# Optimization experiments

Hardware: AMD Instinct MI355X
Metric: run time of the kernel (lower is better)

The kernel has to match this reference:

```python
import jax, jax.numpy as jnp
import numpy as np

COMMITMENT_COST = 0.25


def setup_inputs() -> dict:
    key = jax.random.key(0)
    k1, k2 = jax.random.split(key)
    B, S, D, K = 16, 4096, 256, 4096
    inputs = jax.random.normal(k1, (B, S, D), dtype=jnp.float32)
    # codebook ~ embedding.weight (init scale irrelevant for correctness baseline)
    codebook = jax.random.normal(k2, (K, D), dtype=jnp.float32)
    return {"inputs": inputs, "codebook": codebook}


def reference(inputs, codebook):
    B, S, D = inputs.shape
    flat = inputs.reshape(-1, D)  # (N, D)
    distances = (
        jnp.sum(flat * flat, axis=1, keepdims=True)
        + jnp.sum(codebook * codebook, axis=1)
        - 2.0 * jnp.matmul(flat, codebook.T)
    )
    encoding_indices = jnp.argmin(distances, axis=1)  # (N,)
    quantized = codebook[encoding_indices].reshape(inputs.shape)  # gather
    # commitment loss: beta * mse(inputs, sg(quantized))
    diff = inputs - jax.lax.stop_gradient(quantized)
    commitment_loss = COMMITMENT_COST * jnp.mean(diff * diff)
    # straight-through estimator
    quantized_st = inputs + jax.lax.stop_gradient(quantized - inputs)
    return quantized_st, commitment_loss, encoding_indices
```

## Files before the change

### kernel.cpp

```cpp
#include <hip/hip_runtime.h>
#include <stdint.h>

typedef _Float16 half8 __attribute__((ext_vector_type(8)));
typedef float f32x4 __attribute__((ext_vector_type(4)));

#define DDIM 256
#define KCODES 4096
#define BM 128
#define BN 256
#define NCH 8
#define STEPS 128
#define DELTA 0.02f
#define FLT_BIG 3.4e38f

#define GLOAD_LDS(gsrc, ldst)                                                        \
    __builtin_amdgcn_global_load_lds(                                                \
        (const __attribute__((address_space(1))) void*)(const void*)(gsrc),          \
        (__attribute__((address_space(3))) void*)(void*)(ldst), 16, 0, 0)

__global__ void cvt_hl_kernel(const float* __restrict__ src, half8* __restrict__ dst) {
    int gid = blockIdx.x * 256 + threadIdx.x;
    int p = gid & 7;
    int ch = (gid >> 3) & 7;
    long row = gid >> 6;
    int part = p >> 2, quad = p & 3;
    const float* s = src + row * DDIM + ch * 32 + quad * 8;
    half8 h;
    #pragma unroll
    for (int j = 0; j < 8; ++j) {
        float v = s[j];
        _Float16 hi = (_Float16)v;
        h[j] = part ? (_Float16)(v - (float)hi) : hi;
    }
    dst[gid] = h;
}

__global__ void enorm_kernel(const float* __restrict__ cb, float* __restrict__ en, int K) {
    int gid = blockIdx.x * blockDim.x + threadIdx.x;
    int code = gid >> 6;
    int lane = threadIdx.x & 63;
    if (code >= K) return;
    const float4 v = *reinterpret_cast<const float4*>(&cb[(size_t)code * DDIM + lane * 4]);
    float s = v.x * v.x + v.y * v.y + v.z * v.z + v.w * v.w;
    #pragma unroll
    for (int off = 32; off > 0; off >>= 1) s += __shfl_xor(s, off, 64);
    if (lane == 0) en[code] = s;
}

__global__ __launch_bounds__(512, 2)
void vq_mfma_kernel(const half8* x16, const half8* __restrict__ cb16,
                    const float* __restrict__ en, const float* __restrict__ x,
                    const float* __restrict__ cb, float* out,
                    int* __restrict__ list, int* __restrict__ counter,
                    float* __restrict__ loss_accum, int N) {
    __shared__ __align__(16) half8 Abuf[2][BM * 8];
    __shared__ __align__(16) half8 Bbuf[2][BN * 8];
    __shared__ float en_lds[KCODES];
    __shared__ float red_d[4][BM];
    __shared__ float red_d2[4][BM];
    __shared__ int   red_i[4][BM];
    __shared__ int   binfo[BM];
    __shared__ float wsum[8];

    const int tid = threadIdx.x;
    const int lane = tid & 63;
    const int w = tid >> 6;
    const int wr = w >> 2, wc = w & 3;
    const int l15 = lane & 15, l4 = lane >> 4;
    const int brow = blockIdx.x * BM;
    const size_t ND = (size_t)N * DDIM;

    ((float4*)en_lds)[tid] = ((const float4*)en)[tid];
    ((float4*)en_lds)[tid + 512] = ((const float4*)en)[tid + 512];

    const int lrow = lane >> 3;
    const int swz = (lane & 7) ^ lrow;
    const half8* pA0 = x16 + ((size_t)(brow + w * 8       + lrow) * NCH) * 8 + swz;
    const half8* pA1 = x16 + ((size_t)(brow + (w + 8) * 8 + lrow) * NCH) * 8 + swz;
    const half8* pB0 = cb16 + ((size_t)((w     ) * 8 + lrow) * NCH) * 8 + swz;
    const half8* pB1 = cb16 + ((size_t)((w +  8) * 8 + lrow) * NCH) * 8 + swz;
    const half8* pB2 = cb16 + ((size_t)((w + 16) * 8 + lrow) * NCH) * 8 + swz;
    const half8* pB3 = cb16 + ((size_t)((w + 24) * 8 + lrow) * NCH) * 8 + swz;

#define STAGE(b_) do {                                      \
        GLOAD_LDS(pA0, &Abuf[b_][(w     ) * 64]);           \
        GLOAD_LDS(pA1, &Abuf[b_][(w +  8) * 64]);           \
        GLOAD_LDS(pB0, &Bbuf[b_][(w     ) * 64]);           \
        GLOAD_LDS(pB1, &Bbuf[b_][(w +  8) * 64]);           \
        GLOAD_LDS(pB2, &Bbuf[b_][(w + 16) * 64]);           \
        GLOAD_LDS(pB3, &Bbuf[b_][(w + 24) * 64]);           \
    } while (0)

#define ADVANCE(roll_) do {                                 \
        const int dA = (roll_) ? -56 : 8;                   \
        const int dB = (roll_) ? 16328 : 8;                 \
        pA0 += dA; pA1 += dA;                               \
        pB0 += dB; pB1 += dB; pB2 += dB; pB3 += dB;         \
    } while (0)

    const int sw7 = l15 & 7;
    const _Float16* A0 = (const _Float16*)Abuf;
    const _Float16* B0 = (const _Float16*)Bbuf;
    const _Float16* aH = A0 + wr * 4096 + l15 * 64 + ((l4    ) ^ sw7) * 8;
    const _Float16* aL = A0 + wr * 4096 + l15 * 64 + ((l4 + 4) ^ sw7) * 8;
    const _Float16* bH = B0 + wc * 4096 + l15 * 64 + ((l4    ) ^ sw7) * 8;
    const _Float16* bL = B0 + wc * 4096 + l15 * 64 + ((l4 + 4) ^ sw7) * 8;

    STAGE(0); ADVANCE(0 );

    float bestv[4], best2v[4];
    int bidv[4];
    #pragma unroll
    for (int i = 0; i < 4; ++i) { bestv[i] = FLT_BIG; best2v[i] = FLT_BIG; bidv[i] = 0; }

    const int code_sub = wc * 64 + l4 * 4;
    f32x4 acc[4][4];

    for (int it = 0; it < 16; ++it) {
        #pragma unroll
        for (int m = 0; m < 4; ++m)
            #pragma unroll
            for (int n = 0; n < 4; ++n) acc[m][n] = (f32x4){0.f, 0.f, 0.f, 0.f};

        #pragma unroll
        for (int k = 0; k < 8; ++k) {
            __syncthreads();
            if (k != 7) {
                STAGE((k + 1) & 1);
                ADVANCE(k == 6);
            } else if (it != 15) {
                STAGE(0);
                ADVANCE(0);
            }
            __builtin_amdgcn_sched_barrier(0);

            const int ao = (k & 1) ? 8192 : 0;
            const int bo = (k & 1) ? 16384 : 0;
            half8 ah[4], al[4], bh[4], bl[4];
            #pragma unroll
            for (int i = 0; i < 4; ++i) {
                ah[i] = *(const half8*)(aH + ao + i * 1024);
                al[i] = *(const half8*)(aL + ao + i * 1024);
                bh[i] = *(const half8*)(bH + bo + i * 1024);
                bl[i] = *(const half8*)(bL + bo + i * 1024);
            }
            __builtin_amdgcn_s_setprio(1);
            #pragma unroll
            for (int m = 0; m < 4; ++m)
                #pragma unroll
                for (int n = 0; n < 4; ++n) {
                    acc[m][n] = __builtin_amdgcn_mfma_f32_16x16x32_f16(bh[m], ah[n], acc[m][n], 0, 0, 0);
                    acc[m][n] = __builtin_amdgcn_mfma_f32_16x16x32_f16(bl[m], ah[n], acc[m][n], 0, 0, 0);
                    acc[m][n] = __builtin_amdgcn_mfma_f32_16x16x32_f16(bh[m], al[n], acc[m][n], 0, 0, 0);
                }
            __builtin_amdgcn_s_setprio(0);
        }

        const int c0 = it * BN;
        #pragma unroll
        for (int m = 0; m < 4; ++m) {
            #pragma unroll
            for (int r = 0; r < 4; ++r) {
                int code = c0 + code_sub + m * 16 + r;
                float e = en_lds[code];
                #pragma unroll
                for (int n = 0; n < 4; ++n) {
                    float dist = fmaf(-2.f, acc[m][n][r], e);
                    if (dist < bestv[n]) { best2v[n] = bestv[n]; bestv[n] = dist; bidv[n] = code; }
                    else if (dist < best2v[n]) best2v[n] = dist;
                }
            }
        }
    }
#undef STAGE
#undef ADVANCE

    #pragma unroll
    for (int n = 0; n < 4; ++n) {
        float d = bestv[n], d2 = best2v[n];
        int ix = bidv[n];
        #pragma unroll
        for (int off = 16; off < 64; off <<= 1) {
            float od = __shfl_xor(d, off, 64);
            float od2 = __shfl_xor(d2, off, 64);
            int oi = __shfl_xor(ix, off, 64);
            if (od < d || (od == d && oi < ix)) { d2 = fminf(d, od2); d = od; ix = oi; }
            else d2 = fminf(d2, od);
        }
        if (l4 == 0) {
            int row = wr * 64 + n * 16 + l15;
            red_d[wc][row] = d;
            red_d2[wc][row] = d2;
            red_i[wc][row] = ix;
        }
    }
    __syncthreads();

    if (tid < BM) {
        float d = red_d[0][tid], d2 = red_d2[0][tid];
        int ix = red_i[0][tid];
        #pragma unroll
        for (int q = 1; q < 4; ++q) {
            float od = red_d[q][tid], od2 = red_d2[q][tid];
            int oi = red_i[q][tid];
            if (od < d || (od == d && oi < ix)) { d2 = fminf(d, od2); d = od; ix = oi; }
            else d2 = fminf(d2, od);
        }
        int fl = (d2 - d < DELTA) ? 1 : 0;
        out[ND + 1 + brow + tid] = (float)ix;
        binfo[tid] = ix | (fl << 16);
        if (fl) {
            int pos = atomicAdd(counter, 1);
            list[pos] = brow + tid;
        }
    }
    __syncthreads();

    float lsum = 0.f;
    #pragma unroll 4
    for (int pp = 0; pp < 16; ++pp) {
        int i = tid + pp * 512;
        int row = i >> 6;
        int c4 = (i & 63) << 2;
        int info = binfo[row];
        int code = info & 0xffff;
        const float4 q = *reinterpret_cast<const float4*>(&cb[(size_t)code * DDIM + c4]);
        const float4 xv = *reinterpret_cast<const float4*>(&x[(size_t)(brow + row) * DDIM + c4]);
        float d0 = xv.x - q.x, d1 = xv.y - q.y, d2 = xv.z - q.z, d3 = xv.w - q.w;
        if (!(info >> 16)) lsum += d0 * d0 + d1 * d1 + d2 * d2 + d3 * d3;
        *reinterpret_cast<float4*>(&out[(size_t)(brow + row) * DDIM + c4]) = q;
    }
    #pragma unroll
    for (int off = 32; off > 0; off >>= 1) lsum += __shfl_xor(lsum, off, 64);
    if (lane == 0) wsum[w] = lsum;
    __syncthreads();
    if (tid == 0) {
        float tot = 0.f;
        #pragma unroll
        for (int q = 0; q < 8; ++q) tot += wsum[q];
        atomicAdd(loss_accum, tot * (0.25f / (float)ND));
    }
}

__global__ __launch_bounds__(256)
void rescan_kernel(const float* __restrict__ x, const float* __restrict__ cb,
                   const float* __restrict__ en, const int* __restrict__ list,
                   const int* __restrict__ counter, float* out,
                   float* __restrict__ loss_accum, int N) {
    __shared__ __align__(16) float4 xrow4[64];
    __shared__ float wd[4];
    __shared__ int wi[4];
    __shared__ float wls[4];
    __shared__ int six;
    const int tid = threadIdx.x;
    const int w = tid >> 6;
    const int lane = tid & 63;
    const int cnt = *counter;
    const size_t ND = (size_t)N * DDIM;

    for (int it = blockIdx.x; it < cnt; it += gridDim.x) {
        const int row = list[it];
        __syncthreads();
        if (tid < 64) xrow4[tid] = ((const float4*)&x[(size_t)row * DDIM])[tid];
        __syncthreads();
        const float4 xv = xrow4[lane];
        float bd = FLT_BIG;
        int bi = 0;
        for (int i = 0; i < KCODES / 4; ++i) {
            int code = i * 4 + w;
            const float4 c4 = ((const float4*)&cb[(size_t)code * DDIM])[lane];
            float s = xv.x * c4.x + xv.y * c4.y + xv.z * c4.z + xv.w * c4.w;
            #pragma unroll
            for (int off = 1; off < 64; off <<= 1) s += __shfl_xor(s, off, 64);
            float dist = fmaf(-2.f, s, en[code]);
            if (dist < bd) { bd = dist; bi = code; }
        }
        if (lane == 0) { wd[w] = bd; wi[w] = bi; }
        __syncthreads();
        if (tid == 0) {
            float d = wd[0]; int ix = wi[0];
            #pragma unroll
            for (int q = 1; q < 4; ++q) {
                if (wd[q] < d || (wd[q] == d && wi[q] < ix)) { d = wd[q]; ix = wi[q]; }
            }
            six = ix;
            out[ND + 1 + row] = (float)ix;
        }
        __syncthreads();
        const int ix = six;
        float c = cb[(size_t)ix * DDIM + tid];
        float xs = ((const float*)xrow4)[tid];
        out[(size_t)row * DDIM + tid] = c;
        float dd = xs - c;
        float ss = dd * dd;
        #pragma unroll
        for (int off = 32; off > 0; off >>= 1) ss += __shfl_xor(ss, off, 64);
        if (lane == 0) wls[w] = ss;
        __syncthreads();
        if (tid == 0) {
            float tot = wls[0] + wls[1] + wls[2] + wls[3];
            atomicAdd(loss_accum, tot * (0.25f / (float)ND));
        }
    }
}

__global__ void loss_fin_kernel(const float* __restrict__ loss_accum,
                                float* __restrict__ out, size_t off) {
    if (blockIdx.x == 0 && threadIdx.x == 0) out[off] = *loss_accum;
}

extern "C" void kernel_launch(void* const* d_in, const int* in_sizes, int n_in,
                              void* d_out, int out_size, void* d_ws, size_t ws_size,
                              hipStream_t stream) {
    const float* x = (const float*)d_in[0];
    const float* cb = (const float*)d_in[1];
    const int N = in_sizes[0] / DDIM;
    const int K = in_sizes[1] / DDIM;
    float* out = (float*)d_out;

    half8* x16 = (half8*)d_out;

    half8* cb16 = (half8*)d_ws;
    char* p = (char*)d_ws + (4 << 20);
    float* en = (float*)p;                  p += (size_t)K * 4;
    int* list = (int*)p;                    p += (size_t)N * 4;
    int* counter = (int*)p;                 p += 64;
    float* loss_accum = (float*)p;

    hipMemsetAsync(counter, 0, sizeof(int), stream);
    hipMemsetAsync(loss_accum, 0, sizeof(float), stream);
    cvt_hl_kernel<<<(N * 64) / 256, 256, 0, stream>>>(x, x16);
    cvt_hl_kernel<<<(K * 64) / 256, 256, 0, stream>>>(cb, cb16);
    enorm_kernel<<<(K * 64) / 256, 256, 0, stream>>>(cb, en, K);
    vq_mfma_kernel<<<N / BM, 512, 0, stream>>>(x16, cb16, en, x, cb, out,
                                               list, counter, loss_accum, N);
    rescan_kernel<<<512, 256, 0, stream>>>(x, cb, en, list, counter, out, loss_accum, N);
    loss_fin_kernel<<<1, 64, 0, stream>>>(loss_accum, out, (size_t)N * DDIM);
}
```

Before: 710.6 us.

## Restructure MFMA main loop into ping-pong quadrant schedule with register prefetch

The main GEMM loop is split into four quadrant phases, each running 12 MFMAs. The phases are interleaved with LDS fragment loads and split s_barriers, and the next k-step's A/B fragments are prefetched into registers. Global-to-LDS staging is issued two steps ahead instead of after a full __syncthreads, so memory latency overlaps with matrix math. The hi/lo fp16 split conversion kernel now does one float4 load pair per thread and writes both halves, which halves the thread count. The change raises register pressure and depends on delicate barrier and vmcnt ordering for correctness.

```diff
diff --git a/kernel.cpp b/kernel.cpp
--- a/kernel.cpp
+++ b/kernel.cpp
@@ -9,7 +9,6 @@
 #define BM 128
 #define BN 256
 #define NCH 8
-#define STEPS 128
 #define DELTA 0.02f
 #define FLT_BIG 3.4e38f
 
@@ -20,19 +19,23 @@
 
 __global__ void cvt_hl_kernel(const float* __restrict__ src, half8* __restrict__ dst) {
     int gid = blockIdx.x * 256 + threadIdx.x;
-    int p = gid & 7;
-    int ch = (gid >> 3) & 7;
-    long row = gid >> 6;
-    int part = p >> 2, quad = p & 3;
-    const float* s = src + row * DDIM + ch * 32 + quad * 8;
-    half8 h;
+    int q = gid & 3;
+    int ch = (gid >> 2) & 7;
+    long row = gid >> 5;
+    const float* s = src + row * DDIM + ch * 32 + q * 8;
+    const float4 f0 = ((const float4*)s)[0];
+    const float4 f1 = ((const float4*)s)[1];
+    float vv[8] = {f0.x, f0.y, f0.z, f0.w, f1.x, f1.y, f1.z, f1.w};
+    half8 hi, lo;
     #pragma unroll
     for (int j = 0; j < 8; ++j) {
-        float v = s[j];
-        _Float16 hi = (_Float16)v;
-        h[j] = part ? (_Float16)(v - (float)hi) : hi;
-    }
-    dst[gid] = h;
+        float v = vv[j];
+        _Float16 h = (_Float16)v;
+        hi[j] = h; lo[j] = (_Float16)(v - (float)h);
+    }
+    half8* d = dst + ((row * 8 + ch) << 3);
+    d[q] = hi;
+    d[q + 4] = lo;
 }
 
 __global__ void enorm_kernel(const float* __restrict__ cb, float* __restrict__ en, int K) {
@@ -106,7 +109,18 @@
     const _Float16* bH = B0 + wc * 4096 + l15 * 64 + ((l4    ) ^ sw7) * 8;
     const _Float16* bL = B0 + wc * 4096 + l15 * 64 + ((l4 + 4) ^ sw7) * 8;
 
-    STAGE(0); ADVANCE(0 );
+    STAGE(0); ADVANCE(false);
+    STAGE(1); ADVANCE(false);
+    __syncthreads();
+
+    half8 nah0 = *(const half8*)(aH);
+    half8 nah1 = *(const half8*)(aH + 1024);
+    half8 nal0 = *(const half8*)(aL);
+    half8 nal1 = *(const half8*)(aL + 1024);
+    half8 nbh0 = *(const half8*)(bH);
+    half8 nbh1 = *(const half8*)(bH + 1024);
+    half8 nbl0 = *(const half8*)(bL);
+    half8 nbl1 = *(const half8*)(bL + 1024);
 
     float bestv[4], best2v[4];
     int bidv[4];
@@ -115,6 +129,12 @@
 
     const int code_sub = wc * 64 + l4 * 4;
     f32x4 acc[4][4];
+
+#define TRI(accr, bh_, bl_, ah_, al_) do {                                              \
+        accr = __builtin_amdgcn_mfma_f32_16x16x32_f16(bh_, ah_, accr, 0, 0, 0);         \
+        accr = __builtin_amdgcn_mfma_f32_16x16x32_f16(bl_, ah_, accr, 0, 0, 0);         \
+        accr = __builtin_amdgcn_mfma_f32_16x16x32_f16(bh_, al_, accr, 0, 0, 0);         \
+    } while (0)
 
     for (int it = 0; it < 16; ++it) {
         #pragma unroll
@@ -124,35 +144,64 @@
 
         #pragma unroll
         for (int k = 0; k < 8; ++k) {
-            __syncthreads();
-            if (k != 7) {
-                STAGE((k + 1) & 1);
-                ADVANCE(k == 6);
-            } else if (it != 15) {
-                STAGE(0);
-                ADVANCE(0);
-            }
+            const int ao_c = (k & 1) ? 8192 : 0;
+            const int bo_c = (k & 1) ? 16384 : 0;
+            const int ao_n = (k & 1) ? 0 : 8192;
+            const int bo_n = (k & 1) ? 0 : 16384;
+
+            half8 bh2 = *(const half8*)(bH + bo_c + 2048);
+            half8 bh3 = *(const half8*)(bH + bo_c + 3072);
+            half8 bl2 = *(const half8*)(bL + bo_c + 2048);
+            half8 bl3 = *(const half8*)(bL + bo_c + 3072);
+            __builtin_amdgcn_s_setprio(1);
+            TRI(acc[0][0], nbh0, nbl0, nah0, nal0);
+            TRI(acc[0][1], nbh0, nbl0, nah1, nal1);
+            TRI(acc[1][0], nbh1, nbl1, nah0, nal0);
+            TRI(acc[1][1], nbh1, nbl1, nah1, nal1);
+            __builtin_amdgcn_s_setprio(0);
+            __builtin_amdgcn_s_barrier();
+
+            half8 ah2 = *(const half8*)(aH + ao_c + 2048);
+            half8 ah3 = *(const half8*)(aH + ao_c + 3072);
+            half8 al2 = *(const half8*)(aL + ao_c + 2048);
+            half8 al3 = *(const half8*)(aL + ao_c + 3072);
+            __builtin_amdgcn_s_setprio(1);
+            TRI(acc[2][0], bh2, bl2, nah0, nal0);
+            TRI(acc[2][1], bh2, bl2, nah1, nal1);
+            TRI(acc[3][0], bh3, bl3, nah0, nal0);
+            TRI(acc[3][1], bh3, bl3, nah1, nal1);
+            __builtin_amdgcn_s_setprio(0);
+
+            asm volatile("s_waitcnt vmcnt(0)" ::: "memory");
+            __builtin_amdgcn_s_barrier();
             __builtin_amdgcn_sched_barrier(0);
 
-            const int ao = (k & 1) ? 8192 : 0;
-            const int bo = (k & 1) ? 16384 : 0;
-            half8 ah[4], al[4], bh[4], bl[4];
-            #pragma unroll
-            for (int i = 0; i < 4; ++i) {
-                ah[i] = *(const half8*)(aH + ao + i * 1024);
-                al[i] = *(const half8*)(aL + ao + i * 1024);
-                bh[i] = *(const half8*)(bH + bo + i * 1024);
-                bl[i] = *(const half8*)(bL + bo + i * 1024);
+            if (it < 15 || k < 6) { STAGE(k & 1); ADVANCE(k == 5); }
+            if (it < 15 || k < 7) {
+                nah0 = *(const half8*)(aH + ao_n);
+                nah1 = *(const half8*)(aH + ao_n + 1024);
+                nal0 = *(const half8*)(aL + ao_n);
+                nal1 = *(const half8*)(aL + ao_n + 1024);
             }
             __builtin_amdgcn_s_setprio(1);
-            #pragma unroll
-            for (int m = 0; m < 4; ++m)
-                #pragma unroll
-                for (int n = 0; n < 4; ++n) {
-                    acc[m][n] = __builtin_amdgcn_mfma_f32_16x16x32_f16(bh[m], ah[n], acc[m][n], 0, 0, 0);
-                    acc[m][n] = __builtin_amdgcn_mfma_f32_16x16x32_f16(bl[m], ah[n], acc[m][n], 0, 0, 0);
-                    acc[m][n] = __builtin_amdgcn_mfma_f32_16x16x32_f16(bh[m], al[n], acc[m][n], 0, 0, 0);
-                }
+            TRI(acc[0][2], nbh0, nbl0, ah2, al2);
+            TRI(acc[0][3], nbh0, nbl0, ah3, al3);
+            TRI(acc[1][2], nbh1, nbl1, ah2, al2);
+            TRI(acc[1][3], nbh1, nbl1, ah3, al3);
+            __builtin_amdgcn_s_setprio(0);
+            __builtin_amdgcn_s_barrier();
+
+            if (it < 15 || k < 7) {
+                nbh0 = *(const half8*)(bH + bo_n);
+                nbh1 = *(const half8*)(bH + bo_n + 1024);
+                nbl0 = *(const half8*)(bL + bo_n);
+                nbl1 = *(const half8*)(bL + bo_n + 1024);
+            }
+            __builtin_amdgcn_s_setprio(1);
+            TRI(acc[2][2], bh2, bl2, ah2, al2);
+            TRI(acc[2][3], bh2, bl2, ah3, al3);
+            TRI(acc[3][2], bh3, bl3, ah2, al2);
+            TRI(acc[3][3], bh3, bl3, ah3, al3);
             __builtin_amdgcn_s_setprio(0);
         }
 
@@ -174,6 +223,7 @@
     }
 #undef STAGE
 #undef ADVANCE
+#undef TRI
 
     #pragma unroll
     for (int n = 0; n < 4; ++n) {
@@ -329,8 +379,8 @@
 
     hipMemsetAsync(counter, 0, sizeof(int), stream);
     hipMemsetAsync(loss_accum, 0, sizeof(float), stream);
-    cvt_hl_kernel<<<(N * 64) / 256, 256, 0, stream>>>(x, x16);
-    cvt_hl_kernel<<<(K * 64) / 256, 256, 0, stream>>>(cb, cb16);
+    cvt_hl_kernel<<<(N * 32) / 256, 256, 0, stream>>>(x, x16);
+    cvt_hl_kernel<<<(K * 32) / 256, 256, 0, stream>>>(cb, cb16);
     enorm_kernel<<<(K * 64) / 256, 256, 0, stream>>>(cb, en, K);
     vq_mfma_kernel<<<N / BM, 512, 0, stream>>>(x16, cb16, en, x, cb, out,
                                                list, counter, loss_accum, N);
```

Result: slower. 764.6 us (+7.6%).

## Double row tile to 256 per block and vectorize hi/lo fp16 split conversion

Applied to the files above, without the earlier changes.

Raises the per-block row tile of the split-fp16 MFMA distance GEMM from 128 to 256. Each wave now holds 4x8 accumulators and loads its B fragments once per m across eight A fragments, so every codebook tile streamed into LDS serves twice as many rows. This halves the grid and the total codebook traffic, at the cost of more accumulator registers and fewer blocks, which may lower occupancy under launch_bounds(512,2). The conversion kernel also now reads float4 pairs and writes both hi and lo halves from one thread, halving its thread count.

```diff
diff --git a/kernel.cpp b/kernel.cpp
--- a/kernel.cpp
+++ b/kernel.cpp
@@ -6,10 +6,9 @@
 
 #define DDIM 256
 #define KCODES 4096
-#define BM 128
+#define BM 256
 #define BN 256
 #define NCH 8
-#define STEPS 128
 #define DELTA 0.02f
 #define FLT_BIG 3.4e38f
 
@@ -20,19 +19,23 @@
 
 __global__ void cvt_hl_kernel(const float* __restrict__ src, half8* __restrict__ dst) {
     int gid = blockIdx.x * 256 + threadIdx.x;
-    int p = gid & 7;
-    int ch = (gid >> 3) & 7;
-    long row = gid >> 6;
-    int part = p >> 2, quad = p & 3;
-    const float* s = src + row * DDIM + ch * 32 + quad * 8;
-    half8 h;
+    int q = gid & 3;
+    int ch = (gid >> 2) & 7;
+    long row = gid >> 5;
+    const float* s = src + row * DDIM + ch * 32 + q * 8;
+    const float4 f0 = ((const float4*)s)[0];
+    const float4 f1 = ((const float4*)s)[1];
+    float vv[8] = {f0.x, f0.y, f0.z, f0.w, f1.x, f1.y, f1.z, f1.w};
+    half8 hi, lo;
     #pragma unroll
     for (int j = 0; j < 8; ++j) {
-        float v = s[j];
-        _Float16 hi = (_Float16)v;
-        h[j] = part ? (_Float16)(v - (float)hi) : hi;
-    }
-    dst[gid] = h;
+        float v = vv[j];
+        _Float16 h = (_Float16)v;
+        hi[j] = h; lo[j] = (_Float16)(v - (float)h);
+    }
+    half8* d = dst + ((row * 8 + ch) << 3);
+    d[q] = hi;
+    d[q + 4] = lo;
 }
 
 __global__ void enorm_kernel(const float* __restrict__ cb, float* __restrict__ en, int K) {
@@ -75,16 +78,20 @@
 
     const int lrow = lane >> 3;
     const int swz = (lane & 7) ^ lrow;
-    const half8* pA0 = x16 + ((size_t)(brow + w * 8       + lrow) * NCH) * 8 + swz;
-    const half8* pA1 = x16 + ((size_t)(brow + (w + 8) * 8 + lrow) * NCH) * 8 + swz;
-    const half8* pB0 = cb16 + ((size_t)((w     ) * 8 + lrow) * NCH) * 8 + swz;
-    const half8* pB1 = cb16 + ((size_t)((w +  8) * 8 + lrow) * NCH) * 8 + swz;
-    const half8* pB2 = cb16 + ((size_t)((w + 16) * 8 + lrow) * NCH) * 8 + swz;
-    const half8* pB3 = cb16 + ((size_t)((w + 24) * 8 + lrow) * NCH) * 8 + swz;
+    const half8* pA0 = x16 + (size_t)(brow + (w     ) * 8 + lrow) * 64 + swz;
+    const half8* pA1 = x16 + (size_t)(brow + (w +  8) * 8 + lrow) * 64 + swz;
+    const half8* pA2 = x16 + (size_t)(brow + (w + 16) * 8 + lrow) * 64 + swz;
+    const half8* pA3 = x16 + (size_t)(brow + (w + 24) * 8 + lrow) * 64 + swz;
+    const half8* pB0 = cb16 + (size_t)((w     ) * 8 + lrow) * 64 + swz;
+    const half8* pB1 = cb16 + (size_t)((w +  8) * 8 + lrow) * 64 + swz;
+    const half8* pB2 = cb16 + (size_t)((w + 16) * 8 + lrow) * 64 + swz;
+    const half8* pB3 = cb16 + (size_t)((w + 24) * 8 + lrow) * 64 + swz;
 
 #define STAGE(b_) do {                                      \
         GLOAD_LDS(pA0, &Abuf[b_][(w     ) * 64]);           \
         GLOAD_LDS(pA1, &Abuf[b_][(w +  8) * 64]);           \
+        GLOAD_LDS(pA2, &Abuf[b_][(w + 16) * 64]);           \
+        GLOAD_LDS(pA3, &Abuf[b_][(w + 24) * 64]);           \
         GLOAD_LDS(pB0, &Bbuf[b_][(w     ) * 64]);           \
         GLOAD_LDS(pB1, &Bbuf[b_][(w +  8) * 64]);           \
         GLOAD_LDS(pB2, &Bbuf[b_][(w + 16) * 64]);           \
@@ -94,66 +101,64 @@
 #define ADVANCE(roll_) do {                                 \
         const int dA = (roll_) ? -56 : 8;                   \
         const int dB = (roll_) ? 16328 : 8;                 \
-        pA0 += dA; pA1 += dA;                               \
+        pA0 += dA; pA1 += dA; pA2 += dA; pA3 += dA;         \
         pB0 += dB; pB1 += dB; pB2 += dB; pB3 += dB;         \
     } while (0)
 
     const int sw7 = l15 & 7;
     const _Float16* A0 = (const _Float16*)Abuf;
-    const _Float16* B0 = (const _Float16*)Bbuf;
-    const _Float16* aH = A0 + wr * 4096 + l15 * 64 + ((l4    ) ^ sw7) * 8;
-    const _Float16* aL = A0 + wr * 4096 + l15 * 64 + ((l4 + 4) ^ sw7) * 8;
+    const _Float16* B0 = A0 + 32768;
+    const _Float16* aH = A0 + wr * 8192 + l15 * 64 + ((l4    ) ^ sw7) * 8;
+    const _Float16* aL = A0 + wr * 8192 + l15 * 64 + ((l4 + 4) ^ sw7) * 8;
     const _Float16* bH = B0 + wc * 4096 + l15 * 64 + ((l4    ) ^ sw7) * 8;
     const _Float16* bL = B0 + wc * 4096 + l15 * 64 + ((l4 + 4) ^ sw7) * 8;
 
-    STAGE(0); ADVANCE(0 );
-
-    float bestv[4], best2v[4];
-    int bidv[4];
-    #pragma unroll
-    for (int i = 0; i < 4; ++i) { bestv[i] = FLT_BIG; best2v[i] = FLT_BIG; bidv[i] = 0; }
+    STAGE(0); ADVANCE(false);
+
+    float bestv[8], best2v[8];
+    int bidv[8];
+    #pragma unroll
+    for (int i = 0; i < 8; ++i) { bestv[i] = FLT_BIG; best2v[i] = FLT_BIG; bidv[i] = 0; }
 
     const int code_sub = wc * 64 + l4 * 4;
-    f32x4 acc[4][4];
+    f32x4 acc[4][8];
+
+#define TRI(accr, bh_, bl_, ah_, al_) do {                                              \
+        accr = __builtin_amdgcn_mfma_f32_16x16x32_f16(bh_, ah_, accr, 0, 0, 0);         \
+        accr = __builtin_amdgcn_mfma_f32_16x16x32_f16(bl_, ah_, accr, 0, 0, 0);         \
+        accr = __builtin_amdgcn_mfma_f32_16x16x32_f16(bh_, al_, accr, 0, 0, 0);         \
+    } while (0)
 
     for (int it = 0; it < 16; ++it) {
         #pragma unroll
         for (int m = 0; m < 4; ++m)
             #pragma unroll
-            for (int n = 0; n < 4; ++n) acc[m][n] = (f32x4){0.f, 0.f, 0.f, 0.f};
+            for (int n = 0; n < 8; ++n) acc[m][n] = (f32x4){0.f, 0.f, 0.f, 0.f};
 
         #pragma unroll
         for (int k = 0; k < 8; ++k) {
             __syncthreads();
-            if (k != 7) {
-                STAGE((k + 1) & 1);
-                ADVANCE(k == 6);
-            } else if (it != 15) {
-                STAGE(0);
-                ADVANCE(0);
+            if (k != 7) { STAGE((k + 1) & 1); ADVANCE(k == 6); }
+            else if (it != 15) { STAGE(0); ADVANCE(false); }
+            __builtin_amdgcn_sched_barrier(0);
+
+            const int o = (k & 1) ? 16384 : 0;
+            half8 a_h[8], a_l[8];
+            #pragma unroll
+            for (int n = 0; n < 8; ++n) {
+                a_h[n] = *(const half8*)(aH + o + n * 1024);
+                a_l[n] = *(const half8*)(aL + o + n * 1024);
             }
-            __builtin_amdgcn_sched_barrier(0);
-
-            const int ao = (k & 1) ? 8192 : 0;
-            const int bo = (k & 1) ? 16384 : 0;
-            half8 ah[4], al[4], bh[4], bl[4];
-            #pragma unroll
-            for (int i = 0; i < 4; ++i) {
-                ah[i] = *(const half8*)(aH + ao + i * 1024);
-                al[i] = *(const half8*)(aL + ao + i * 1024);
-                bh[i] = *(const half8*)(bH + bo + i * 1024);
-                bl[i] = *(const half8*)(bL + bo + i * 1024);
+            #pragma unroll
+            for (int m = 0; m < 4; ++m) {
+                half8 bh = *(const half8*)(bH + o + m * 1024);
+                half8 bl = *(const half8*)(bL + o + m * 1024);
+                __builtin_amdgcn_s_setprio(1);
+                #pragma unroll
+                for (int n = 0; n < 8; ++n)
+                    TRI(acc[m][n], bh, bl, a_h[n], a_l[n]);
+                __builtin_amdgcn_s_setprio(0);
             }
-            __builtin_amdgcn_s_setprio(1);
-            #pragma unroll
-            for (int m = 0; m < 4; ++m)
-                #pragma unroll
-                for (int n = 0; n < 4; ++n) {
-                    acc[m][n] = __builtin_amdgcn_mfma_f32_16x16x32_f16(bh[m], ah[n], acc[m][n], 0, 0, 0);
-                    acc[m][n] = __builtin_amdgcn_mfma_f32_16x16x32_f16(bl[m], ah[n], acc[m][n], 0, 0, 0);
-                    acc[m][n] = __builtin_amdgcn_mfma_f32_16x16x32_f16(bh[m], al[n], acc[m][n], 0, 0, 0);
-                }
-            __builtin_amdgcn_s_setprio(0);
         }
 
         const int c0 = it * BN;
@@ -164,7 +169,7 @@
                 int code = c0 + code_sub + m * 16 + r;
                 float e = en_lds[code];
                 #pragma unroll
-                for (int n = 0; n < 4; ++n) {
+                for (int n = 0; n < 8; ++n) {
                     float dist = fmaf(-2.f, acc[m][n][r], e);
                     if (dist < bestv[n]) { best2v[n] = bestv[n]; bestv[n] = dist; bidv[n] = code; }
                     else if (dist < best2v[n]) best2v[n] = dist;
@@ -174,9 +179,10 @@
     }
 #undef STAGE
 #undef ADVANCE
-
-    #pragma unroll
-    for (int n = 0; n < 4; ++n) {
+#undef TRI
+
+    #pragma unroll
+    for (int n = 0; n < 8; ++n) {
         float d = bestv[n], d2 = best2v[n];
         int ix = bidv[n];
         #pragma unroll
@@ -188,7 +194,7 @@
             else d2 = fminf(d2, od);
         }
         if (l4 == 0) {
-            int row = wr * 64 + n * 16 + l15;
+            int row = wr * 128 + n * 16 + l15;
             red_d[wc][row] = d;
             red_d2[wc][row] = d2;
             red_i[wc][row] = ix;
@@ -218,7 +224,7 @@
 
     float lsum = 0.f;
     #pragma unroll 4
-    for (int pp = 0; pp < 16; ++pp) {
+    for (int pp = 0; pp < 32; ++pp) {
         int i = tid + pp * 512;
         int row = i >> 6;
         int c4 = (i & 63) << 2;
@@ -329,8 +335,8 @@
 
     hipMemsetAsync(counter, 0, sizeof(int), stream);
     hipMemsetAsync(loss_accum, 0, sizeof(float), stream);
-    cvt_hl_kernel<<<(N * 64) / 256, 256, 0, stream>>>(x, x16);
-    cvt_hl_kernel<<<(K * 64) / 256, 256, 0, stream>>>(cb, cb16);
+    cvt_hl_kernel<<<(N * 32) / 256, 256, 0, stream>>>(x, x16);
+    cvt_hl_kernel<<<(K * 32) / 256, 256, 0, stream>>>(cb, cb16);
     enorm_kernel<<<(K * 64) / 256, 256, 0, stream>>>(cb, en, K);
     vq_mfma_kernel<<<N / BM, 512, 0, stream>>>(x16, cb16, en, x, cb, out,
                                                list, counter, loss_accum, N);
```

Result: slower. 758.4 us (+6.7%).

## Keep split-fp16 input rows in registers and stream codebook fragments directly

Applied to the files above, without the earlier changes.

The main kernel now loads a 64-row tile of fp32 inputs into LDS once and converts it in-kernel into hi/lo fp16 register fragments, so the separate input conversion pass and its extra global traffic go away. Each of the 8 waves then scans its own 512-code slice of a pre-packed MFMA-ready codebook straight from global memory into registers. This removes the double-buffered LDS staging and the per-step block barriers. The cross-wave argmin reduction grows from 4 to 8 partials. In exchange the kernel needs heavy register pressure for the resident A fragments (64 half8 values), gets no LDS reuse of codebook tiles across waves, and halves the rows per block, which doubles total codebook reads from L2.

```diff
diff --git a/kernel.cpp b/kernel.cpp
--- a/kernel.cpp
+++ b/kernel.cpp
@@ -6,10 +6,7 @@
 
 #define DDIM 256
 #define KCODES 4096
-#define BM 128
-#define BN 256
-#define NCH 8
-#define STEPS 128
+#define BM 64
 #define DELTA 0.02f
 #define FLT_BIG 3.4e38f
 
@@ -18,21 +15,26 @@
         (const __attribute__((address_space(1))) void*)(const void*)(gsrc),          \
         (__attribute__((address_space(3))) void*)(void*)(ldst), 16, 0, 0)
 
-__global__ void cvt_hl_kernel(const float* __restrict__ src, half8* __restrict__ dst) {
+__global__ void cvt_cb_kernel(const float* __restrict__ cb, half8* __restrict__ cbp) {
     int gid = blockIdx.x * 256 + threadIdx.x;
-    int p = gid & 7;
-    int ch = (gid >> 3) & 7;
-    long row = gid >> 6;
-    int part = p >> 2, quad = p & 3;
-    const float* s = src + row * DDIM + ch * 32 + quad * 8;
-    half8 h;
+    int l = gid & 63;
+    int k = (gid >> 6) & 7;
+    int g = gid >> 9;
+    int code = g * 16 + (l & 15);
+    int quad = (l >> 4) & 3;
+    const float* s = cb + (size_t)code * DDIM + k * 32 + quad * 8;
+    float4 f0 = ((const float4*)s)[0];
+    float4 f1 = ((const float4*)s)[1];
+    float ff[8] = {f0.x, f0.y, f0.z, f0.w, f1.x, f1.y, f1.z, f1.w};
+    half8 hv, lv;
     #pragma unroll
     for (int j = 0; j < 8; ++j) {
-        float v = s[j];
-        _Float16 hi = (_Float16)v;
-        h[j] = part ? (_Float16)(v - (float)hi) : hi;
-    }
-    dst[gid] = h;
+        float v = ff[j];
+        _Float16 h = (_Float16)v;
+        hv[j] = h; lv[j] = (_Float16)(v - (float)h);
+    }
+    cbp[(size_t)(g * 8 + k) * 128 + l] = hv;
+    cbp[(size_t)(g * 8 + k) * 128 + 64 + l] = lv;
 }
 
 __global__ void enorm_kernel(const float* __restrict__ cb, float* __restrict__ en, int K) {
@@ -48,24 +50,21 @@
 }
 
 __global__ __launch_bounds__(512, 2)
-void vq_mfma_kernel(const half8* x16, const half8* __restrict__ cb16,
-                    const float* __restrict__ en, const float* __restrict__ x,
-                    const float* __restrict__ cb, float* out,
-                    int* __restrict__ list, int* __restrict__ counter,
+void vq_mfma_kernel(const float* __restrict__ x, const half8* __restrict__ cbp,
+                    const float* __restrict__ en, const float* __restrict__ cb,
+                    float* out, int* __restrict__ list, int* __restrict__ counter,
                     float* __restrict__ loss_accum, int N) {
-    __shared__ __align__(16) half8 Abuf[2][BM * 8];
-    __shared__ __align__(16) half8 Bbuf[2][BN * 8];
+    __shared__ __align__(16) float xs[BM * DDIM];
     __shared__ float en_lds[KCODES];
-    __shared__ float red_d[4][BM];
-    __shared__ float red_d2[4][BM];
-    __shared__ int   red_i[4][BM];
+    __shared__ float red_d[8][BM];
+    __shared__ float red_d2[8][BM];
+    __shared__ int   red_i[8][BM];
     __shared__ int   binfo[BM];
     __shared__ float wsum[8];
 
     const int tid = threadIdx.x;
     const int lane = tid & 63;
     const int w = tid >> 6;
-    const int wr = w >> 2, wc = w & 3;
     const int l15 = lane & 15, l4 = lane >> 4;
     const int brow = blockIdx.x * BM;
     const size_t ND = (size_t)N * DDIM;
@@ -73,107 +72,82 @@
     ((float4*)en_lds)[tid] = ((const float4*)en)[tid];
     ((float4*)en_lds)[tid + 512] = ((const float4*)en)[tid + 512];
 
-    const int lrow = lane >> 3;
-    const int swz = (lane & 7) ^ lrow;
-    const half8* pA0 = x16 + ((size_t)(brow + w * 8       + lrow) * NCH) * 8 + swz;
-    const half8* pA1 = x16 + ((size_t)(brow + (w + 8) * 8 + lrow) * NCH) * 8 + swz;
-    const half8* pB0 = cb16 + ((size_t)((w     ) * 8 + lrow) * NCH) * 8 + swz;
-    const half8* pB1 = cb16 + ((size_t)((w +  8) * 8 + lrow) * NCH) * 8 + swz;
-    const half8* pB2 = cb16 + ((size_t)((w + 16) * 8 + lrow) * NCH) * 8 + swz;
-    const half8* pB3 = cb16 + ((size_t)((w + 24) * 8 + lrow) * NCH) * 8 + swz;
-
-#define STAGE(b_) do {                                      \
-        GLOAD_LDS(pA0, &Abuf[b_][(w     ) * 64]);           \
-        GLOAD_LDS(pA1, &Abuf[b_][(w +  8) * 64]);           \
-        GLOAD_LDS(pB0, &Bbuf[b_][(w     ) * 64]);           \
-        GLOAD_LDS(pB1, &Bbuf[b_][(w +  8) * 64]);           \
-        GLOAD_LDS(pB2, &Bbuf[b_][(w + 16) * 64]);           \
-        GLOAD_LDS(pB3, &Bbuf[b_][(w + 24) * 64]);           \
-    } while (0)
-
-#define ADVANCE(roll_) do {                                 \
-        const int dA = (roll_) ? -56 : 8;                   \
-        const int dB = (roll_) ? 16328 : 8;                 \
-        pA0 += dA; pA1 += dA;                               \
-        pB0 += dB; pB1 += dB; pB2 += dB; pB3 += dB;         \
-    } while (0)
-
-    const int sw7 = l15 & 7;
-    const _Float16* A0 = (const _Float16*)Abuf;
-    const _Float16* B0 = (const _Float16*)Bbuf;
-    const _Float16* aH = A0 + wr * 4096 + l15 * 64 + ((l4    ) ^ sw7) * 8;
-    const _Float16* aL = A0 + wr * 4096 + l15 * 64 + ((l4 + 4) ^ sw7) * 8;
-    const _Float16* bH = B0 + wc * 4096 + l15 * 64 + ((l4    ) ^ sw7) * 8;
-    const _Float16* bL = B0 + wc * 4096 + l15 * 64 + ((l4 + 4) ^ sw7) * 8;
-
-    STAGE(0); ADVANCE(0 );
+    #pragma unroll
+    for (int i = 0; i < 8; ++i) {
+        const int row = i * 8 + w;
+        const float* src = x + (size_t)(brow + row) * DDIM + ((lane ^ w) << 2);
+        GLOAD_LDS(src, xs + row * DDIM + (lane << 2));
+    }
+    __syncthreads();
+
+    half8 ahf[4][8], alf[4][8];
+    const int s7 = l15 & 7;
+    #pragma unroll
+    for (int n = 0; n < 4; ++n) {
+        const float* base = xs + (n * 16 + l15) * DDIM;
+        #pragma unroll
+        for (int k = 0; k < 8; ++k) {
+            int c0 = (k * 8 + l4 * 2) ^ s7;
+            float4 f0 = *(const float4*)(base + c0 * 4);
+            float4 f1 = *(const float4*)(base + (c0 ^ 1) * 4);
+            float ff[8] = {f0.x, f0.y, f0.z, f0.w, f1.x, f1.y, f1.z, f1.w};
+            half8 hv, lv;
+            #pragma unroll
+            for (int j = 0; j < 8; ++j) {
+                float v = ff[j];
+                _Float16 h = (_Float16)v;
+                hv[j] = h; lv[j] = (_Float16)(v - (float)h);
+            }
+            ahf[n][k] = hv; alf[n][k] = lv;
+        }
+    }
 
     float bestv[4], best2v[4];
     int bidv[4];
     #pragma unroll
     for (int i = 0; i < 4; ++i) { bestv[i] = FLT_BIG; best2v[i] = FLT_BIG; bidv[i] = 0; }
 
-    const int code_sub = wc * 64 + l4 * 4;
-    f32x4 acc[4][4];
-
-    for (int it = 0; it < 16; ++it) {
-        #pragma unroll
-        for (int m = 0; m < 4; ++m)
-            #pragma unroll
-            for (int n = 0; n < 4; ++n) acc[m][n] = (f32x4){0.f, 0.f, 0.f, 0.f};
-
+#define TRI(accr, bh_, bl_, ah_, al_) do {                                              \
+        accr = __builtin_amdgcn_mfma_f32_16x16x32_f16(bh_, ah_, accr, 0, 0, 0);         \
+        accr = __builtin_amdgcn_mfma_f32_16x16x32_f16(bl_, ah_, accr, 0, 0, 0);         \
+        accr = __builtin_amdgcn_mfma_f32_16x16x32_f16(bh_, al_, accr, 0, 0, 0);         \
+    } while (0)
+
+    const half8* pb = cbp + (size_t)w * 32768 + lane;
+    int gbase = w * 512;
+
+    for (int gi = 0; gi < 32; ++gi) {
+        half8 bh[8], bl[8];
         #pragma unroll
         for (int k = 0; k < 8; ++k) {
-            __syncthreads();
-            if (k != 7) {
-                STAGE((k + 1) & 1);
-                ADVANCE(k == 6);
-            } else if (it != 15) {
-                STAGE(0);
-                ADVANCE(0);
+            bh[k] = pb[k * 128];
+            bl[k] = pb[k * 128 + 64];
+        }
+        f32x4 acc[4];
+        #pragma unroll
+        for (int n = 0; n < 4; ++n) acc[n] = (f32x4){0.f, 0.f, 0.f, 0.f};
+        #pragma unroll
+        for (int k = 0; k < 8; ++k) {
+            #pragma unroll
+            for (int n = 0; n < 4; ++n)
+                TRI(acc[n], bh[k], bl[k], ahf[n][k], alf[n][k]);
+        }
+        float4 e4 = *(const float4*)(en_lds + gbase + l4 * 4);
+        #pragma unroll
+        for (int r = 0; r < 4; ++r) {
+            int code = gbase + l4 * 4 + r;
+            float e = (r == 0) ? e4.x : (r == 1) ? e4.y : (r == 2) ? e4.z : e4.w;
+            #pragma unroll
+            for (int n = 0; n < 4; ++n) {
+                float dist = fmaf(-2.f, acc[n][r], e);
+                if (dist < bestv[n]) { best2v[n] = bestv[n]; bestv[n] = dist; bidv[n] = code; }
+                else if (dist < best2v[n]) best2v[n] = dist;
             }
-            __builtin_amdgcn_sched_barrier(0);
-
-            const int ao = (k & 1) ? 8192 : 0;
-            const int bo = (k & 1) ? 16384 : 0;
-            half8 ah[4], al[4], bh[4], bl[4];
-            #pragma unroll
-            for (int i = 0; i < 4; ++i) {
-                ah[i] = *(const half8*)(aH + ao + i * 1024);
-                al[i] = *(const half8*)(aL + ao + i * 1024);
-                bh[i] = *(const half8*)(bH + bo + i * 1024);
-                bl[i] = *(const half8*)(bL + bo + i * 1024);
-            }
-            __builtin_amdgcn_s_setprio(1);
-            #pragma unroll
-            for (int m = 0; m < 4; ++m)
-                #pragma unroll
-                for (int n = 0; n < 4; ++n) {
-                    acc[m][n] = __builtin_amdgcn_mfma_f32_16x16x32_f16(bh[m], ah[n], acc[m][n], 0, 0, 0);
-                    acc[m][n] = __builtin_amdgcn_mfma_f32_16x16x32_f16(bl[m], ah[n], acc[m][n], 0, 0, 0);
-                    acc[m][n] = __builtin_amdgcn_mfma_f32_16x16x32_f16(bh[m], al[n], acc[m][n], 0, 0, 0);
-                }
-            __builtin_amdgcn_s_setprio(0);
-        }
-
-        const int c0 = it * BN;
-        #pragma unroll
-        for (int m = 0; m < 4; ++m) {
-            #pragma unroll
-            for (int r = 0; r < 4; ++r) {
-                int code = c0 + code_sub + m * 16 + r;
-                float e = en_lds[code];
-                #pragma unroll
-                for (int n = 0; n < 4; ++n) {
-                    float dist = fmaf(-2.f, acc[m][n][r], e);
-                    if (dist < bestv[n]) { best2v[n] = bestv[n]; bestv[n] = dist; bidv[n] = code; }
-                    else if (dist < best2v[n]) best2v[n] = dist;
-                }
-            }
-        }
-    }
-#undef STAGE
-#undef ADVANCE
+        }
+        pb += 1024;
+        gbase += 16;
+    }
+#undef TRI
 
     #pragma unroll
     for (int n = 0; n < 4; ++n) {
@@ -188,10 +162,10 @@
             else d2 = fminf(d2, od);
         }
         if (l4 == 0) {
-            int row = wr * 64 + n * 16 + l15;
-            red_d[wc][row] = d;
-            red_d2[wc][row] = d2;
-            red_i[wc][row] = ix;
+            int row = n * 16 + l15;
+            red_d[w][row] = d;
+            red_d2[w][row] = d2;
+            red_i[w][row] = ix;
         }
     }
     __syncthreads();
@@ -200,7 +174,7 @@
         float d = red_d[0][tid], d2 = red_d2[0][tid];
         int ix = red_i[0][tid];
         #pragma unroll
-        for (int q = 1; q < 4; ++q) {
+        for (int q = 1; q < 8; ++q) {
             float od = red_d[q][tid], od2 = red_d2[q][tid];
             int oi = red_i[q][tid];
             if (od < d || (od == d && oi < ix)) { d2 = fminf(d, od2); d = od; ix = oi; }
@@ -217,8 +191,8 @@
     __syncthreads();
 
     float lsum = 0.f;
-    #pragma unroll 4
-    for (int pp = 0; pp < 16; ++pp) {
+    #pragma unroll
+    for (int pp = 0; pp < 8; ++pp) {
         int i = tid + pp * 512;
         int row = i >> 6;
         int c4 = (i & 63) << 2;
@@ -289,9 +263,9 @@
         __syncthreads();
         const int ix = six;
         float c = cb[(size_t)ix * DDIM + tid];
-        float xs = ((const float*)xrow4)[tid];
+        float xs_ = ((const float*)xrow4)[tid];
         out[(size_t)row * DDIM + tid] = c;
-        float dd = xs - c;
+        float dd = xs_ - c;
         float ss = dd * dd;
         #pragma unroll
         for (int off = 32; off > 0; off >>= 1) ss += __shfl_xor(ss, off, 64);
@@ -318,9 +292,7 @@
     const int K = in_sizes[1] / DDIM;
     float* out = (float*)d_out;
 
-    half8* x16 = (half8*)d_out;
-
-    half8* cb16 = (half8*)d_ws;
+    half8* cbp = (half8*)d_ws;
     char* p = (char*)d_ws + (4 << 20);
     float* en = (float*)p;                  p += (size_t)K * 4;
     int* list = (int*)p;                    p += (size_t)N * 4;
@@ -329,10 +301,9 @@
 
     hipMemsetAsync(counter, 0, sizeof(int), stream);
     hipMemsetAsync(loss_accum, 0, sizeof(float), stream);
-    cvt_hl_kernel<<<(N * 64) / 256, 256, 0, stream>>>(x, x16);
-    cvt_hl_kernel<<<(K * 64) / 256, 256, 0, stream>>>(cb, cb16);
+    cvt_cb_kernel<<<(K * 32) / 256, 256, 0, stream>>>(cb, cbp);
     enorm_kernel<<<(K * 64) / 256, 256, 0, stream>>>(cb, en, K);
-    vq_mfma_kernel<<<N / BM, 512, 0, stream>>>(x16, cb16, en, x, cb, out,
+    vq_mfma_kernel<<<N / BM, 512, 0, stream>>>(x, cbp, en, cb, out,
                                                list, counter, loss_accum, N);
     rescan_kernel<<<512, 256, 0, stream>>>(x, cb, en, list, counter, out, loss_accum, N);
     loss_fin_kernel<<<1, 64, 0, stream>>>(loss_accum, out, (size_t)N * DDIM);
```

New measurement: 1.118 ms. +57.4%, slower.
